# Performance work log

Hardware: AMD Instinct MI355X
Metric: run time of the kernel (lower is better)

Reference implementation:

```python
import jax, jax.numpy as jnp
import numpy as np

EPS = 1e-5  # BatchNorm eps (torch default)

def _bn(x, gamma, beta):
    # training-mode BatchNorm over the edge/node (leading) axis, biased var
    mean = x.mean(axis=0, keepdims=True)
    var = x.var(axis=0, keepdims=True)
    return (x - mean) * jax.lax.rsqrt(var + EPS) * gamma + beta

def _silu(x):
    return x * jax.nn.sigmoid(x)

def setup_inputs() -> dict:
    N, E, H, NH = 50000, 800000, 128, 4
    HD = H // NH
    key = jax.random.key(0)
    ks = jax.random.split(key, 8)
    x = jax.random.normal(ks[0], (N, H), dtype=jnp.float32)
    weight = jax.random.uniform(ks[1], (N, 1), dtype=jnp.float32)  # positive fraction weights
    src = jax.random.randint(ks[2], (E,), 0, N)
    dst = jax.random.randint(ks[3], (E,), 0, N)
    # f: Linear(2H, 1) + BN(1)
    Wf = jax.random.normal(ks[4], (2 * H, 1), dtype=jnp.float32) * 0.05
    bf = jnp.zeros((1,), jnp.float32)
    f_gamma = jnp.ones((1,), jnp.float32)
    f_beta = jnp.zeros((1,), jnp.float32)
    # g: NH heads of Linear(2H, HD) + BN(HD), stacked on leading head axis
    Wg = jax.random.normal(ks[5], (NH, 2 * H, HD), dtype=jnp.float32) * 0.05
    bg = jnp.zeros((NH, HD), jnp.float32)
    g_gamma = jnp.ones((NH, HD), jnp.float32)
    g_beta = jnp.zeros((NH, HD), jnp.float32)
    # bn_nodes: BN(H)
    n_gamma = jnp.ones((H,), jnp.float32)
    n_beta = jnp.zeros((H,), jnp.float32)
    return dict(x=x, weight=weight, src=src, dst=dst, Wf=Wf, bf=bf,
                f_gamma=f_gamma, f_beta=f_beta, Wg=Wg, bg=bg,
                g_gamma=g_gamma, g_beta=g_beta, n_gamma=n_gamma, n_beta=n_beta)

def reference(x, weight, src, dst, Wf, bf, f_gamma, f_beta, Wg, bg, g_gamma, g_beta, n_gamma, n_beta):
    N = x.shape[0]
    E = src.shape[0]
    # per-edge concat of src/dst node features: [E, 2H]
    hihj = jnp.concatenate([x[src], x[dst]], axis=-1)
    # attention logit f(hihj) = SiLU(BN(Linear)) then exp: [E, 1]
    exp_e = jnp.exp(_silu(_bn(hihj @ Wf + bf, f_gamma, f_beta)))
    # weighted softmax-like normalization over incoming edges of each dst node
    we = weight[src] * exp_e                                   # [E, 1]
    sum_w_exp = jax.ops.segment_sum(we, dst, num_segments=N)   # [N, 1]
    a = we / sum_w_exp[dst]                                    # [E, 1]
    # multi-head message: a_ij * SiLU(BN(Linear_h(hihj))) per head, concat
    z = jnp.einsum('ed,hdk->ehk', hihj, Wg) + bg               # [E, NH, HD]
    z = _silu(_bn(z, g_gamma, g_beta))
    msg = (a[:, :, None] * z).reshape(E, -1)                   # [E, H]
    h = jax.ops.segment_sum(msg, dst, num_segments=N)          # [N, H]
    out = _bn(h, n_gamma, n_beta) + x                          # residual
    return out
```

## Files before the change

### kernel.cpp

```cpp
#include <hip/hip_runtime.h>
#include <hip/hip_bf16.h>
#include <math.h>

#define HDIM 128
#define PAD 64
typedef unsigned short ushort_t;
typedef unsigned int uint_t;
typedef __attribute__((ext_vector_type(8))) short bf16x8;
typedef __attribute__((ext_vector_type(4))) float f32x4;
typedef __attribute__((ext_vector_type(2))) float v2f;

__device__ __forceinline__ float wave_allreduce(float v){
  #pragma unroll
  for (int o = 1; o < 64; o <<= 1) v += __shfl_xor(v, o);
  return v;
}

__device__ __forceinline__ ushort_t f2bf(float f){
  uint_t u = __float_as_uint(f);
  uint_t r = (u + 0x7fffu + ((u >> 16) & 1u)) >> 16;
  return (ushort_t)r;
}

__device__ __forceinline__ v2f bf2(uint_t u){
  v2f r;
  r.x = __uint_as_float(u << 16);
  r.y = __uint_as_float(u & 0xffff0000u);
  return r;
}

__global__ __launch_bounds__(128) void k_wpack(const float* __restrict__ Wg,
    const float* __restrict__ Wf, ushort_t* __restrict__ W2t,
    int* __restrict__ cnt, int N){
  int b = blockIdx.x;
  int k = threadIdx.x;
  if (b < 272){
    float val;
    if (b < 128)       val = Wg[(size_t)(b >> 5) * 8192 + k * 32 + (b & 31)];
    else if (b < 256){ int c2 = b - 128;
                       val = Wg[(size_t)(c2 >> 5) * 8192 + (k + 128) * 32 + (c2 & 31)]; }
    else if (b == 256) val = Wf[k];
    else if (b == 257) val = Wf[128 + k];
    else               val = 0.f;
    W2t[(size_t)b * 128 + k] = f2bf(val);
  } else {
    int i = (b - 272) * 128 + k;
    if (i < N) cnt[i] = 0;
  }
}

__global__ __launch_bounds__(256) void k_gemmfill(const float* __restrict__ x,
    const ushort_t* __restrict__ W2t, const float* __restrict__ weight,
    ushort_t* __restrict__ Pb, ushort_t* __restrict__ Qb,
    float* __restrict__ v, float2* __restrict__ uw2,
    const int* __restrict__ src, const int* __restrict__ dst,
    int* __restrict__ cnt, int* __restrict__ es,
    int N, int E, int GB){
  if ((int)blockIdx.x < GB){
    int wid = __builtin_amdgcn_readfirstlane(threadIdx.x >> 6);
    int lane = threadIdx.x & 63;
    int quad = lane >> 4, col = lane & 15;
    int strip = blockIdx.x * 2 + (wid >> 1);
    int half = wid & 1;
    int n_base = strip * 16;
    if (n_base >= N) return;
    int tbeg = half * 8;
    int ntile = half ? 9 : 8;
    f32x4 acc[9];
    #pragma unroll
    for (int t = 0; t < 9; ++t) acc[t] = (f32x4){0.f, 0.f, 0.f, 0.f};
    int row = n_base + col;
    int rowc = row < N ? row : N - 1;
    const float* xr = x + (size_t)rowc * HDIM + quad * 8;
    #pragma unroll
    for (int kk = 0; kk < 4; ++kk){
      float4 a0 = *(const float4*)(xr + kk * 32);
      float4 a1 = *(const float4*)(xr + kk * 32 + 4);
      bf16x8 af;
      af[0] = (short)f2bf(a0.x); af[1] = (short)f2bf(a0.y);
      af[2] = (short)f2bf(a0.z); af[3] = (short)f2bf(a0.w);
      af[4] = (short)f2bf(a1.x); af[5] = (short)f2bf(a1.y);
      af[6] = (short)f2bf(a1.z); af[7] = (short)f2bf(a1.w);
      const ushort_t* wb = W2t + (size_t)(tbeg * 16) * 128 + (size_t)col * 128 + kk * 32 + quad * 8;
      #pragma unroll
      for (int t = 0; t < 9; ++t){
        if (t < ntile){
          bf16x8 bfr = *(const bf16x8*)(wb + (size_t)t * 16 * 128);
          acc[t] = __builtin_amdgcn_mfma_f32_16x16x32_bf16(af, bfr, acc[t], 0, 0, 0);
        }
      }
    }
    #pragma unroll
    for (int t = 0; t < 8; ++t){
      int ct = tbeg + t;
      int c = ct * 16 + col;
      #pragma unroll
      for (int r = 0; r < 4; ++r){
        int n = n_base + quad * 4 + r;
        if (n < N){
          ushort_t valb = f2bf(acc[t][r]);
          if (c < 128) Pb[(size_t)n * HDIM + c] = valb;
          else         Qb[(size_t)n * HDIM + (c - 128)] = valb;
        }
      }
    }
    if (half){
      #pragma unroll
      for (int r = 0; r < 4; ++r){
        int n = n_base + quad * 4 + r;
        if (n < N){
          float val = acc[8][r];
          if (col == 0)      uw2[n] = make_float2(val, weight[n]);
          else if (col == 1) v[n] = val;
        }
      }
    }
  } else {
    int bi = blockIdx.x - GB;
    int part = bi & 7;
    int nch = (gridDim.x - GB) >> 3;
    int chunk = bi >> 3;
    int Npp = (N + 7) >> 3;
    int lo = part * Npp;
    int hi = lo + Npp; if (hi > N) hi = N;
    int stride = nch * 256;
    for (int e = chunk * 256 + threadIdx.x; e < E; e += stride){
      int d = dst[e];
      if (d >= lo && d < hi){
        int c = atomicAdd(&cnt[d], 1);
        if (c < PAD) es[(size_t)d * PAD + c] = src[e];
      }
    }
  }
}

__global__ __launch_bounds__(256) void k_gstats(const ushort_t* __restrict__ Pb,
    const ushort_t* __restrict__ Qb, const float* __restrict__ v,
    const float2* __restrict__ uw2, const int* __restrict__ es,
    const int* __restrict__ cnt, float* __restrict__ pstatG, int N, int NW){
  int lane = threadIdx.x & 63;
  int wid = __builtin_amdgcn_readfirstlane(threadIdx.x >> 6);
  int wg = blockIdx.x * 4 + wid;
  const uint_t* Pu = (const uint_t*)Pb;
  const uint_t* Qu = (const uint_t*)Qb;
  v2f gs = {0.f, 0.f}, gq = {0.f, 0.f};
  float fs = 0.f, fq = 0.f;
  for (int n = wg; n < N; n += NW){
    int dn = cnt[n]; dn = dn < PAD ? dn : PAD;
    v2f q = bf2(Qu[(size_t)n * 64 + lane]);
    float vn = v[n];
    int sj = 0;
    if (lane < dn){
      sj = es[(size_t)n * PAD + lane];
      float t = uw2[sj].x + vn;
      fs += t; fq = fmaf(t, t, fq);
    }
    int j = 0;
    for (; j + 3 < dn; j += 4){
      int s0 = __shfl(sj, j),     s1 = __shfl(sj, j + 1);
      int s2 = __shfl(sj, j + 2), s3 = __shfl(sj, j + 3);
      uint_t p0 = Pu[(size_t)s0 * 64 + lane];
      uint_t p1 = Pu[(size_t)s1 * 64 + lane];
      uint_t p2 = Pu[(size_t)s2 * 64 + lane];
      uint_t p3 = Pu[(size_t)s3 * 64 + lane];
      v2f y0 = bf2(p0) + q, y1 = bf2(p1) + q, y2 = bf2(p2) + q, y3 = bf2(p3) + q;
      gs += y0 + y1 + y2 + y3;
      gq += y0 * y0; gq += y1 * y1; gq += y2 * y2; gq += y3 * y3;
    }
    for (; j < dn; ++j){
      int s0 = __shfl(sj, j);
      v2f y0 = bf2(Pu[(size_t)s0 * 64 + lane]) + q;
      gs += y0; gq += y0 * y0;
    }
  }
  fs = wave_allreduce(fs); fq = wave_allreduce(fq);
  float* pb = pstatG + (size_t)wg * 258;
  *(float2*)&pb[2 * lane]       = make_float2(gs.x, gs.y);
  *(float2*)&pb[128 + 2 * lane] = make_float2(gq.x, gq.y);
  if (lane == 0){ pb[256] = fs; pb[257] = fq; }
}

__global__ __launch_bounds__(256) void k_redfin1(const float* __restrict__ pstatG,
    int NW, const float* __restrict__ g_gamma, const float* __restrict__ g_beta,
    const float* __restrict__ f_gamma, const float* __restrict__ f_beta,
    float* __restrict__ fin, long long E){
  int j = blockIdx.x;
  int c1 = (j < 128) ? j : 256;
  int c2 = (j < 128) ? 128 + j : 257;
  double s1 = 0, s2 = 0;
  for (int b = threadIdx.x; b < NW; b += 256){
    const float* pb = pstatG + (size_t)b * 258;
    s1 += (double)pb[c1]; s2 += (double)pb[c2];
  }
  __shared__ double m1[256], m2[256];
  m1[threadIdx.x] = s1; m2[threadIdx.x] = s2;
  __syncthreads();
  for (int o = 128; o; o >>= 1){
    if (threadIdx.x < o){ m1[threadIdx.x] += m1[threadIdx.x + o];
                          m2[threadIdx.x] += m2[threadIdx.x + o]; }
    __syncthreads();
  }
  if (threadIdx.x == 0){
    double m = m1[0] / (double)E;
    double var = m2[0] / (double)E - m * m;
    if (j < 128){
      float sc = (float)((double)g_gamma[j] / sqrt(var + 1e-5));
      fin[2 + j] = sc; fin[130 + j] = g_beta[j] - (float)m * sc;
    } else {
      float sc = (float)((double)f_gamma[0] / sqrt(var + 1e-5));
      fin[0] = sc; fin[1] = f_beta[0] - (float)m * sc;
    }
  }
}

__global__ __launch_bounds__(256) void k_msg(const ushort_t* __restrict__ Pb,
    const ushort_t* __restrict__ Qb, const float* __restrict__ v,
    const float2* __restrict__ uw2, const int* __restrict__ es,
    const int* __restrict__ cnt, const float* __restrict__ fin,
    float* __restrict__ h, float* __restrict__ pstatH, int N, int NW){
  int lane = threadIdx.x & 63;
  int wid = __builtin_amdgcn_readfirstlane(threadIdx.x >> 6);
  int wg = blockIdx.x * 4 + wid;
  const uint_t* Pu = (const uint_t*)Pb;
  const uint_t* Qu = (const uint_t*)Qb;
  float fsc = fin[0], fsh = fin[1];
  v2f gsc = {fin[2 + 2 * lane], fin[3 + 2 * lane]};
  v2f gsh = {fin[130 + 2 * lane], fin[131 + 2 * lane]};
  v2f hs = {0.f, 0.f}, hq = {0.f, 0.f};
  for (int n = wg; n < N; n += NW){
    int dn = cnt[n]; dn = dn < PAD ? dn : PAD;
    float vn = v[n];
    int sj = 0; float wj = 0.f;
    if (lane < dn){
      sj = es[(size_t)n * PAD + lane];
      float2 uw = uw2[sj];
      float t = fmaf(uw.x + vn, fsc, fsh);
      float sl = t * __builtin_amdgcn_rcpf(1.f + __expf(-t));
      wj = uw.y * __expf(sl);
    }
    float sw = wave_allreduce(wj);
    wj *= (dn > 0) ? (1.f / sw) : 0.f;
    v2f q = bf2(Qu[(size_t)n * 64 + lane]);
    v2f acc = {0.f, 0.f};
    int j = 0;
    for (; j + 3 < dn; j += 4){
      int s0 = __shfl(sj, j),     s1 = __shfl(sj, j + 1);
      int s2 = __shfl(sj, j + 2), s3 = __shfl(sj, j + 3);
      float a0 = __shfl(wj, j),     a1 = __shfl(wj, j + 1);
      float a2 = __shfl(wj, j + 2), a3 = __shfl(wj, j + 3);
      uint_t p0 = Pu[(size_t)s0 * 64 + lane];
      uint_t p1 = Pu[(size_t)s1 * 64 + lane];
      uint_t p2 = Pu[(size_t)s2 * 64 + lane];
      uint_t p3 = Pu[(size_t)s3 * 64 + lane];
      {
        v2f y = (bf2(p0) + q) * gsc + gsh;
        float e0 = __expf(-y.x), e1 = __expf(-y.y);
        float d0 = 1.f + e0, d1 = 1.f + e1;
        float r = __builtin_amdgcn_rcpf(d0 * d1) * a0;
        v2f z; z.x = y.x * d1; z.y = y.y * d0;
        acc += z * (v2f){r, r};
      }
      {
        v2f y = (bf2(p1) + q) * gsc + gsh;
        float e0 = __expf(-y.x), e1 = __expf(-y.y);
        float d0 = 1.f + e0, d1 = 1.f + e1;
        float r = __builtin_amdgcn_rcpf(d0 * d1) * a1;
        v2f z; z.x = y.x * d1; z.y = y.y * d0;
        acc += z * (v2f){r, r};
      }
      {
        v2f y = (bf2(p2) + q) * gsc + gsh;
        float e0 = __expf(-y.x), e1 = __expf(-y.y);
        float d0 = 1.f + e0, d1 = 1.f + e1;
        float r = __builtin_amdgcn_rcpf(d0 * d1) * a2;
        v2f z; z.x = y.x * d1; z.y = y.y * d0;
        acc += z * (v2f){r, r};
      }
      {
        v2f y = (bf2(p3) + q) * gsc + gsh;
        float e0 = __expf(-y.x), e1 = __expf(-y.y);
        float d0 = 1.f + e0, d1 = 1.f + e1;
        float r = __builtin_amdgcn_rcpf(d0 * d1) * a3;
        v2f z; z.x = y.x * d1; z.y = y.y * d0;
        acc += z * (v2f){r, r};
      }
    }
    for (; j < dn; ++j){
      int s0 = __shfl(sj, j);
      float a0 = __shfl(wj, j);
      v2f y = (bf2(Pu[(size_t)s0 * 64 + lane]) + q) * gsc + gsh;
      float e0 = __expf(-y.x), e1 = __expf(-y.y);
      float d0 = 1.f + e0, d1 = 1.f + e1;
      float r = __builtin_amdgcn_rcpf(d0 * d1) * a0;
      v2f z; z.x = y.x * d1; z.y = y.y * d0;
      acc += z * (v2f){r, r};
    }
    *(float2*)&h[(size_t)n * 128 + 2 * lane] = make_float2(acc.x, acc.y);
    hs += acc; hq += acc * acc;
  }
  float* pb = pstatH + (size_t)wg * 256;
  *(float2*)&pb[2 * lane]       = make_float2(hs.x, hs.y);
  *(float2*)&pb[128 + 2 * lane] = make_float2(hq.x, hq.y);
}

__global__ __launch_bounds__(256) void k_redfin2(const float* __restrict__ pstatH,
    int NW, const float* __restrict__ n_gamma, const float* __restrict__ n_beta,
    float* __restrict__ fin, int N){
  int j = blockIdx.x;
  double s1 = 0, s2 = 0;
  for (int b = threadIdx.x; b < NW; b += 256){
    const float* pb = pstatH + (size_t)b * 256;
    s1 += (double)pb[j]; s2 += (double)pb[128 + j];
  }
  __shared__ double m1[256], m2[256];
  m1[threadIdx.x] = s1; m2[threadIdx.x] = s2;
  __syncthreads();
  for (int o = 128; o; o >>= 1){
    if (threadIdx.x < o){ m1[threadIdx.x] += m1[threadIdx.x + o];
                          m2[threadIdx.x] += m2[threadIdx.x + o]; }
    __syncthreads();
  }
  if (threadIdx.x == 0){
    double m = m1[0] / (double)N;
    double var = m2[0] / (double)N - m * m;
    float sc = (float)((double)n_gamma[j] / sqrt(var + 1e-5));
    fin[258 + j] = sc; fin[386 + j] = n_beta[j] - (float)m * sc;
  }
}

__global__ __launch_bounds__(256) void k_out(const float* __restrict__ h,
    const float* __restrict__ x, const float* __restrict__ fin,
    float* __restrict__ out, int total4){
  int i = blockIdx.x * 256 + threadIdx.x;
  if (i >= total4) return;
  const float4* h4 = (const float4*)h; const float4* x4 = (const float4*)x;
  float4 hv = h4[i], xv = x4[i];
  int c = (i * 4) & 127;
  float4 o;
  o.x = fmaf(hv.x, fin[258 + c],     fin[386 + c])     + xv.x;
  o.y = fmaf(hv.y, fin[258 + c + 1], fin[386 + c + 1]) + xv.y;
  o.z = fmaf(hv.z, fin[258 + c + 2], fin[386 + c + 2]) + xv.z;
  o.w = fmaf(hv.w, fin[258 + c + 3], fin[386 + c + 3]) + xv.w;
  ((float4*)out)[i] = o;
}

extern "C" void kernel_launch(void* const* d_in, const int* in_sizes, int n_in,
                              void* d_out, int out_size, void* d_ws, size_t ws_size,
                              hipStream_t stream){
  const float* x       = (const float*)d_in[0];
  const float* weight  = (const float*)d_in[1];
  const int*   src     = (const int*)d_in[2];
  const int*   dst     = (const int*)d_in[3];
  const float* Wf      = (const float*)d_in[4];
  const float* f_gamma = (const float*)d_in[6];
  const float* f_beta  = (const float*)d_in[7];
  const float* Wg      = (const float*)d_in[8];
  const float* g_gamma = (const float*)d_in[10];
  const float* g_beta  = (const float*)d_in[11];
  const float* n_gamma = (const float*)d_in[12];
  const float* n_beta  = (const float*)d_in[13];
  float* out = (float*)d_out;

  int N = in_sizes[0] / HDIM;
  int E = in_sizes[2];

  char* ws = (char*)d_ws;
  size_t off = 0;
  auto alloc = [&](size_t bytes)->char*{
    char* p = ws + off; off = (off + bytes + 255) & ~(size_t)255; return p;
  };
  ushort_t* Pb    = (ushort_t*)alloc((size_t)N * HDIM * 2);
  ushort_t* Qb    = (ushort_t*)alloc((size_t)N * HDIM * 2);
  float* h        = (float*)alloc((size_t)N * HDIM * 4);
  float* v        = (float*)alloc((size_t)N * 4);
  float2* uw2     = (float2*)alloc((size_t)N * 8);
  int* es         = (int*)alloc((size_t)N * PAD * 4);
  ushort_t* W2t   = (ushort_t*)alloc((size_t)272 * 128 * 2);
  int* cnt        = (int*)alloc((size_t)N * 4);
  const int NWB = 2048;
  const int NW  = NWB * 4;
  float*  pstatG = (float*)alloc((size_t)NW * 258 * 4);
  float*  pstatH = (float*)alloc((size_t)NW * 256 * 4);
  float*  fin    = (float*)alloc(514 * 4);

  int GB = (N + 31) / 32;
  const int FB = 4096;

  k_wpack   <<<272 + (N + 127) / 128, 128, 0, stream>>>(Wg, Wf, W2t, cnt, N);
  k_gemmfill<<<GB + FB, 256, 0, stream>>>(x, W2t, weight, Pb, Qb, v, uw2,
                                          src, dst, cnt, es, N, E, GB);
  k_gstats  <<<NWB, 256, 0, stream>>>(Pb, Qb, v, uw2, es, cnt, pstatG, N, NW);
  k_redfin1 <<<129, 256, 0, stream>>>(pstatG, NW, g_gamma, g_beta, f_gamma, f_beta, fin, (long long)E);
  k_msg     <<<NWB, 256, 0, stream>>>(Pb, Qb, v, uw2, es, cnt, fin, h, pstatH, N, NW);
  k_redfin2 <<<128, 256, 0, stream>>>(pstatH, NW, n_gamma, n_beta, fin, N);
  k_out     <<<(N * HDIM / 4 + 255) / 256, 256, 0, stream>>>(h, x, fin, out, N * HDIM / 4);
}
```

Measured before the change: 302.4 us.

## Partition node loops by XCD, prefetch next node, unroll gathers, block-reduce stats

Both edge-gather kernels now assign each block to one of eight contiguous node partitions, matching the partitioned edge fill, so each XCD's L2 sees a localized node range. Per-node metadata for the next node (count, edge list, Q row, v) is prefetched while the current node runs. The gather loop is unrolled to 8 edges. Softmax normalization is deferred until after accumulation, and per-wave statistics are combined in shared memory so one partial per block is written. The goal is to hide gather latency and shrink the reduction inputs, at the cost of more registers and possible load imbalance across partitions.

```diff
diff --git a/kernel.cpp b/kernel.cpp
--- a/kernel.cpp
+++ b/kernel.cpp
@@ -137,58 +137,89 @@
 __global__ __launch_bounds__(256) void k_gstats(const ushort_t* __restrict__ Pb,
     const ushort_t* __restrict__ Qb, const float* __restrict__ v,
     const float2* __restrict__ uw2, const int* __restrict__ es,
-    const int* __restrict__ cnt, float* __restrict__ pstatG, int N, int NW){
+    const int* __restrict__ cnt, float* __restrict__ pstatG, int N, int GB){
   int lane = threadIdx.x & 63;
   int wid = __builtin_amdgcn_readfirstlane(threadIdx.x >> 6);
-  int wg = blockIdx.x * 4 + wid;
+  int part = ((int)blockIdx.x - GB) & 7;
+  int Npp = (N + 7) >> 3;
+  int lo = part * Npp;
+  int hi = lo + Npp; if (hi > N) hi = N;
+  int step = (gridDim.x >> 3) << 2;
   const uint_t* Pu = (const uint_t*)Pb;
   const uint_t* Qu = (const uint_t*)Qb;
   v2f gs = {0.f, 0.f}, gq = {0.f, 0.f};
   float fs = 0.f, fq = 0.f;
-  for (int n = wg; n < N; n += NW){
-    int dn = cnt[n]; dn = dn < PAD ? dn : PAD;
-    v2f q = bf2(Qu[(size_t)n * 64 + lane]);
-    float vn = v[n];
-    int sj = 0;
+  int n = lo + ((blockIdx.x >> 3) << 2) + wid;
+  int dnA = 0, sjA = 0; uint_t qA = 0; float vA = 0.f;
+  if (n < hi){
+    dnA = cnt[n];
+    sjA = es[(size_t)n * PAD + lane];
+    qA  = Qu[(size_t)n * 64 + lane];
+    vA  = v[n];
+  }
+  while (n < hi){
+    int nn = n + step;
+    int dnB = 0, sjB = 0; uint_t qB = 0; float vB = 0.f;
+    if (nn < hi){
+      dnB = cnt[nn];
+      sjB = es[(size_t)nn * PAD + lane];
+      qB  = Qu[(size_t)nn * 64 + lane];
+      vB  = v[nn];
+    }
+    int dn = dnA < PAD ? dnA : PAD;
+    int sj = sjA;
     if (lane < dn){
-      sj = es[(size_t)n * PAD + lane];
-      float t = uw2[sj].x + vn;
+      float2 uw = uw2[sj];
+      float t = uw.x + vA;
       fs += t; fq = fmaf(t, t, fq);
     }
+    v2f q = bf2(qA);
     int j = 0;
+#define GSTAT(p) { v2f y = bf2(p) + q; gs += y; \
+                   gq.x = fmaf(y.x, y.x, gq.x); gq.y = fmaf(y.y, y.y, gq.y); }
+    for (; j + 7 < dn; j += 8){
+      int s0=__shfl(sj,j),   s1=__shfl(sj,j+1), s2=__shfl(sj,j+2), s3=__shfl(sj,j+3);
+      int s4=__shfl(sj,j+4), s5=__shfl(sj,j+5), s6=__shfl(sj,j+6), s7=__shfl(sj,j+7);
+      uint_t p0=Pu[(size_t)s0*64+lane], p1=Pu[(size_t)s1*64+lane];
+      uint_t p2=Pu[(size_t)s2*64+lane], p3=Pu[(size_t)s3*64+lane];
+      uint_t p4=Pu[(size_t)s4*64+lane], p5=Pu[(size_t)s5*64+lane];
+      uint_t p6=Pu[(size_t)s6*64+lane], p7=Pu[(size_t)s7*64+lane];
+      GSTAT(p0) GSTAT(p1) GSTAT(p2) GSTAT(p3)
+      GSTAT(p4) GSTAT(p5) GSTAT(p6) GSTAT(p7)
+    }
     for (; j + 3 < dn; j += 4){
-      int s0 = __shfl(sj, j),     s1 = __shfl(sj, j + 1);
-      int s2 = __shfl(sj, j + 2), s3 = __shfl(sj, j + 3);
-      uint_t p0 = Pu[(size_t)s0 * 64 + lane];
-      uint_t p1 = Pu[(size_t)s1 * 64 + lane];
-      uint_t p2 = Pu[(size_t)s2 * 64 + lane];
-      uint_t p3 = Pu[(size_t)s3 * 64 + lane];
-      v2f y0 = bf2(p0) + q, y1 = bf2(p1) + q, y2 = bf2(p2) + q, y3 = bf2(p3) + q;
-      gs += y0 + y1 + y2 + y3;
-      gq += y0 * y0; gq += y1 * y1; gq += y2 * y2; gq += y3 * y3;
+      int s0=__shfl(sj,j), s1=__shfl(sj,j+1), s2=__shfl(sj,j+2), s3=__shfl(sj,j+3);
+      uint_t p0=Pu[(size_t)s0*64+lane], p1=Pu[(size_t)s1*64+lane];
+      uint_t p2=Pu[(size_t)s2*64+lane], p3=Pu[(size_t)s3*64+lane];
+      GSTAT(p0) GSTAT(p1) GSTAT(p2) GSTAT(p3)
     }
     for (; j < dn; ++j){
       int s0 = __shfl(sj, j);
-      v2f y0 = bf2(Pu[(size_t)s0 * 64 + lane]) + q;
-      gs += y0; gq += y0 * y0;
-    }
+      uint_t p0 = Pu[(size_t)s0*64+lane];
+      GSTAT(p0)
+    }
+#undef GSTAT
+    n = nn; dnA = dnB; sjA = sjB; qA = qB; vA = vB;
   }
   fs = wave_allreduce(fs); fq = wave_allreduce(fq);
-  float* pb = pstatG + (size_t)wg * 258;
-  *(float2*)&pb[2 * lane]       = make_float2(gs.x, gs.y);
-  *(float2*)&pb[128 + 2 * lane] = make_float2(gq.x, gq.y);
-  if (lane == 0){ pb[256] = fs; pb[257] = fq; }
+  __shared__ float red[4][258];
+  red[wid][2*lane]       = gs.x; red[wid][2*lane+1]   = gs.y;
+  red[wid][128+2*lane]   = gq.x; red[wid][129+2*lane] = gq.y;
+  if (lane == 0){ red[wid][256] = fs; red[wid][257] = fq; }
+  __syncthreads();
+  for (int c = threadIdx.x; c < 258; c += 256)
+    pstatG[(size_t)blockIdx.x * 258 + c] = red[0][c] + red[1][c] + red[2][c] + red[3][c];
 }
 
 __global__ __launch_bounds__(256) void k_redfin1(const float* __restrict__ pstatG,
-    int NW, const float* __restrict__ g_gamma, const float* __restrict__ g_beta,
+    int NB, const float* __restrict__ g_gamma, const float* __restrict__ g_beta,
     const float* __restrict__ f_gamma, const float* __restrict__ f_beta,
     float* __restrict__ fin, long long E){
   int j = blockIdx.x;
   int c1 = (j < 128) ? j : 256;
   int c2 = (j < 128) ? 128 + j : 257;
   double s1 = 0, s2 = 0;
-  for (int b = threadIdx.x; b < NW; b += 256){
+  for (int b = threadIdx.x; b < NB; b += 256){
     const float* pb = pstatG + (size_t)b * 258;
     s1 += (double)pb[c1]; s2 += (double)pb[c2];
   }
@@ -217,98 +248,101 @@
     const ushort_t* __restrict__ Qb, const float* __restrict__ v,
     const float2* __restrict__ uw2, const int* __restrict__ es,
     const int* __restrict__ cnt, const float* __restrict__ fin,
-    float* __restrict__ h, float* __restrict__ pstatH, int N, int NW){
+    float* __restrict__ h, float* __restrict__ pstatH, int N, int GB){
   int lane = threadIdx.x & 63;
   int wid = __builtin_amdgcn_readfirstlane(threadIdx.x >> 6);
-  int wg = blockIdx.x * 4 + wid;
+  int part = ((int)blockIdx.x - GB) & 7;
+  int Npp = (N + 7) >> 3;
+  int lo = part * Npp;
+  int hi = lo + Npp; if (hi > N) hi = N;
+  int step = (gridDim.x >> 3) << 2;
   const uint_t* Pu = (const uint_t*)Pb;
   const uint_t* Qu = (const uint_t*)Qb;
   float fsc = fin[0], fsh = fin[1];
-  v2f gsc = {fin[2 + 2 * lane], fin[3 + 2 * lane]};
-  v2f gsh = {fin[130 + 2 * lane], fin[131 + 2 * lane]};
+  v2f gsc = {fin[2 + 2*lane], fin[3 + 2*lane]};
+  v2f gsh = {fin[130 + 2*lane], fin[131 + 2*lane]};
   v2f hs = {0.f, 0.f}, hq = {0.f, 0.f};
-  for (int n = wg; n < N; n += NW){
-    int dn = cnt[n]; dn = dn < PAD ? dn : PAD;
-    float vn = v[n];
-    int sj = 0; float wj = 0.f;
+  int n = lo + ((blockIdx.x >> 3) << 2) + wid;
+  int dnA = 0, sjA = 0; uint_t qA = 0; float vA = 0.f;
+  if (n < hi){
+    dnA = cnt[n];
+    sjA = es[(size_t)n * PAD + lane];
+    qA  = Qu[(size_t)n * 64 + lane];
+    vA  = v[n];
+  }
+  while (n < hi){
+    int nn = n + step;
+    int dnB = 0, sjB = 0; uint_t qB = 0; float vB = 0.f;
+    if (nn < hi){
+      dnB = cnt[nn];
+      sjB = es[(size_t)nn * PAD + lane];
+      qB  = Qu[(size_t)nn * 64 + lane];
+      vB  = v[nn];
+    }
+    int dn = dnA < PAD ? dnA : PAD;
+    int sj = sjA;
+    float wj = 0.f;
     if (lane < dn){
-      sj = es[(size_t)n * PAD + lane];
       float2 uw = uw2[sj];
-      float t = fmaf(uw.x + vn, fsc, fsh);
-      float sl = t * __builtin_amdgcn_rcpf(1.f + __expf(-t));
+      float tt = fmaf(uw.x + vA, fsc, fsh);
+      float sl = tt * __builtin_amdgcn_rcpf(1.f + __expf(-tt));
       wj = uw.y * __expf(sl);
     }
-    float sw = wave_allreduce(wj);
-    wj *= (dn > 0) ? (1.f / sw) : 0.f;
-    v2f q = bf2(Qu[(size_t)n * 64 + lane]);
+    v2f q = bf2(qA);
     v2f acc = {0.f, 0.f};
     int j = 0;
+#define EDGE(p,a) { v2f y = (bf2(p) + q) * gsc + gsh; \
+      float e0 = __expf(-y.x), e1 = __expf(-y.y); \
+      float d0 = 1.f + e0, d1 = 1.f + e1; \
+      float r = __builtin_amdgcn_rcpf(d0 * d1) * a; \
+      acc.x = fmaf(y.x * d1, r, acc.x); acc.y = fmaf(y.y * d0, r, acc.y); }
+    for (; j + 7 < dn; j += 8){
+      int s0=__shfl(sj,j),   s1=__shfl(sj,j+1), s2=__shfl(sj,j+2), s3=__shfl(sj,j+3);
+      int s4=__shfl(sj,j+4), s5=__shfl(sj,j+5), s6=__shfl(sj,j+6), s7=__shfl(sj,j+7);
+      float a0=__shfl(wj,j),   a1=__shfl(wj,j+1), a2=__shfl(wj,j+2), a3=__shfl(wj,j+3);
+      float a4=__shfl(wj,j+4), a5=__shfl(wj,j+5), a6=__shfl(wj,j+6), a7=__shfl(wj,j+7);
+      uint_t p0=Pu[(size_t)s0*64+lane], p1=Pu[(size_t)s1*64+lane];
+      uint_t p2=Pu[(size_t)s2*64+lane], p3=Pu[(size_t)s3*64+lane];
+      uint_t p4=Pu[(size_t)s4*64+lane], p5=Pu[(size_t)s5*64+lane];
+      uint_t p6=Pu[(size_t)s6*64+lane], p7=Pu[(size_t)s7*64+lane];
+      EDGE(p0,a0) EDGE(p1,a1) EDGE(p2,a2) EDGE(p3,a3)
+      EDGE(p4,a4) EDGE(p5,a5) EDGE(p6,a6) EDGE(p7,a7)
+    }
     for (; j + 3 < dn; j += 4){
-      int s0 = __shfl(sj, j),     s1 = __shfl(sj, j + 1);
-      int s2 = __shfl(sj, j + 2), s3 = __shfl(sj, j + 3);
-      float a0 = __shfl(wj, j),     a1 = __shfl(wj, j + 1);
-      float a2 = __shfl(wj, j + 2), a3 = __shfl(wj, j + 3);
-      uint_t p0 = Pu[(size_t)s0 * 64 + lane];
-      uint_t p1 = Pu[(size_t)s1 * 64 + lane];
-      uint_t p2 = Pu[(size_t)s2 * 64 + lane];
-      uint_t p3 = Pu[(size_t)s3 * 64 + lane];
-      {
-        v2f y = (bf2(p0) + q) * gsc + gsh;
-        float e0 = __expf(-y.x), e1 = __expf(-y.y);
-        float d0 = 1.f + e0, d1 = 1.f + e1;
-        float r = __builtin_amdgcn_rcpf(d0 * d1) * a0;
-        v2f z; z.x = y.x * d1; z.y = y.y * d0;
-        acc += z * (v2f){r, r};
-      }
-      {
-        v2f y = (bf2(p1) + q) * gsc + gsh;
-        float e0 = __expf(-y.x), e1 = __expf(-y.y);
-        float d0 = 1.f + e0, d1 = 1.f + e1;
-        float r = __builtin_amdgcn_rcpf(d0 * d1) * a1;
-        v2f z; z.x = y.x * d1; z.y = y.y * d0;
-        acc += z * (v2f){r, r};
-      }
-      {
-        v2f y = (bf2(p2) + q) * gsc + gsh;
-        float e0 = __expf(-y.x), e1 = __expf(-y.y);
-        float d0 = 1.f + e0, d1 = 1.f + e1;
-        float r = __builtin_amdgcn_rcpf(d0 * d1) * a2;
-        v2f z; z.x = y.x * d1; z.y = y.y * d0;
-        acc += z * (v2f){r, r};
-      }
-      {
-        v2f y = (bf2(p3) + q) * gsc + gsh;
-        float e0 = __expf(-y.x), e1 = __expf(-y.y);
-        float d0 = 1.f + e0, d1 = 1.f + e1;
-        float r = __builtin_amdgcn_rcpf(d0 * d1) * a3;
-        v2f z; z.x = y.x * d1; z.y = y.y * d0;
-        acc += z * (v2f){r, r};
-      }
+      int s0=__shfl(sj,j), s1=__shfl(sj,j+1), s2=__shfl(sj,j+2), s3=__shfl(sj,j+3);
+      float a0=__shfl(wj,j), a1=__shfl(wj,j+1), a2=__shfl(wj,j+2), a3=__shfl(wj,j+3);
+      uint_t p0=Pu[(size_t)s0*64+lane], p1=Pu[(size_t)s1*64+lane];
+      uint_t p2=Pu[(size_t)s2*64+lane], p3=Pu[(size_t)s3*64+lane];
+      EDGE(p0,a0) EDGE(p1,a1) EDGE(p2,a2) EDGE(p3,a3)
     }
     for (; j < dn; ++j){
       int s0 = __shfl(sj, j);
       float a0 = __shfl(wj, j);
-      v2f y = (bf2(Pu[(size_t)s0 * 64 + lane]) + q) * gsc + gsh;
-      float e0 = __expf(-y.x), e1 = __expf(-y.y);
-      float d0 = 1.f + e0, d1 = 1.f + e1;
-      float r = __builtin_amdgcn_rcpf(d0 * d1) * a0;
-      v2f z; z.x = y.x * d1; z.y = y.y * d0;
-      acc += z * (v2f){r, r};
-    }
-    *(float2*)&h[(size_t)n * 128 + 2 * lane] = make_float2(acc.x, acc.y);
+      uint_t p0 = Pu[(size_t)s0*64+lane];
+      EDGE(p0,a0)
+    }
+#undef EDGE
+    float sw = wave_allreduce(wj);
+    float rs = (dn > 0) ? (1.f / sw) : 0.f;
+    acc.x *= rs; acc.y *= rs;
+    *(float2*)&h[(size_t)n * 128 + 2*lane] = make_float2(acc.x, acc.y);
     hs += acc; hq += acc * acc;
-  }
-  float* pb = pstatH + (size_t)wg * 256;
-  *(float2*)&pb[2 * lane]       = make_float2(hs.x, hs.y);
-  *(float2*)&pb[128 + 2 * lane] = make_float2(hq.x, hq.y);
+    n = nn; dnA = dnB; sjA = sjB; qA = qB; vA = vB;
+  }
+  __shared__ float red[4][256];
+  red[wid][2*lane]       = hs.x; red[wid][2*lane+1]   = hs.y;
+  red[wid][128+2*lane]   = hq.x; red[wid][129+2*lane] = hq.y;
+  __syncthreads();
+  int c = threadIdx.x;
+  pstatH[(size_t)blockIdx.x * 256 + c] = red[0][c] + red[1][c] + red[2][c] + red[3][c];
 }
 
 __global__ __launch_bounds__(256) void k_redfin2(const float* __restrict__ pstatH,
-    int NW, const float* __restrict__ n_gamma, const float* __restrict__ n_beta,
+    int NB, const float* __restrict__ n_gamma, const float* __restrict__ n_beta,
     float* __restrict__ fin, int N){
   int j = blockIdx.x;
   double s1 = 0, s2 = 0;
-  for (int b = threadIdx.x; b < NW; b += 256){
+  for (int b = threadIdx.x; b < NB; b += 256){
     const float* pb = pstatH + (size_t)b * 256;
     s1 += (double)pb[j]; s2 += (double)pb[128 + j];
   }
@@ -378,9 +412,9 @@
   ushort_t* W2t   = (ushort_t*)alloc((size_t)272 * 128 * 2);
   int* cnt        = (int*)alloc((size_t)N * 4);
   const int NWB = 2048;
-  const int NW  = NWB * 4;
-  float*  pstatG = (float*)alloc((size_t)NW * 258 * 4);
-  float*  pstatH = (float*)alloc((size_t)NW * 256 * 4);
+  const int NB  = NWB;
+  float*  pstatG = (float*)alloc((size_t)NB * 258 * 4);
+  float*  pstatH = (float*)alloc((size_t)NB * 256 * 4);
   float*  fin    = (float*)alloc(514 * 4);
 
   int GB = (N + 31) / 32;
@@ -389,9 +423,9 @@
   k_wpack   <<<272 + (N + 127) / 128, 128, 0, stream>>>(Wg, Wf, W2t, cnt, N);
   k_gemmfill<<<GB + FB, 256, 0, stream>>>(x, W2t, weight, Pb, Qb, v, uw2,
                                           src, dst, cnt, es, N, E, GB);
-  k_gstats  <<<NWB, 256, 0, stream>>>(Pb, Qb, v, uw2, es, cnt, pstatG, N, NW);
-  k_redfin1 <<<129, 256, 0, stream>>>(pstatG, NW, g_gamma, g_beta, f_gamma, f_beta, fin, (long long)E);
-  k_msg     <<<NWB, 256, 0, stream>>>(Pb, Qb, v, uw2, es, cnt, fin, h, pstatH, N, NW);
-  k_redfin2 <<<128, 256, 0, stream>>>(pstatH, NW, n_gamma, n_beta, fin, N);
+  k_gstats  <<<NWB, 256, 0, stream>>>(Pb, Qb, v, uw2, es, cnt, pstatG, N, GB);
+  k_redfin1 <<<129, 256, 0, stream>>>(pstatG, NB, g_gamma, g_beta, f_gamma, f_beta, fin, (long long)E);
+  k_msg     <<<NWB, 256, 0, stream>>>(Pb, Qb, v, uw2, es, cnt, fin, h, pstatH, N, GB);
+  k_redfin2 <<<128, 256, 0, stream>>>(pstatH, NB, n_gamma, n_beta, fin, N);
   k_out     <<<(N * HDIM / 4 + 255) / 256, 256, 0, stream>>>(h, x, fin, out, N * HDIM / 4);
 }
```

Result: faster. 273.9 us (-9.4%).
